# Kernel optimization log

Hardware: AMD Instinct MI355X
Metric: run time of the kernel (lower is better)

Reference implementation:

```python
import jax, jax.numpy as jnp
import numpy as np

CORE_DIM = 128
MEMORY_SLOTS = 64
B, S = 4, 4096


def setup_inputs() -> dict:
    key = jax.random.key(0)
    k1, k2, k3, k4, k5 = jax.random.split(key, 5)
    x = jax.random.normal(k1, (B, S, CORE_DIM), dtype=jnp.float32)
    memory_keys = jax.random.normal(k2, (MEMORY_SLOTS, CORE_DIM), dtype=jnp.float32)
    memory_ops = jax.random.normal(k3, (MEMORY_SLOTS, CORE_DIM, CORE_DIM), dtype=jnp.float32)
    # nn.Linear(core_dim, core_dim): weight [out, in], bias [out]
    bound = 1.0 / np.sqrt(CORE_DIM)
    Wq = jax.random.uniform(k4, (CORE_DIM, CORE_DIM), minval=-bound, maxval=bound, dtype=jnp.float32)
    bq = jax.random.uniform(k5, (CORE_DIM,), minval=-bound, maxval=bound, dtype=jnp.float32)
    return {"input_tensor": x, "memory_keys": memory_keys, "memory_ops": memory_ops, "Wq": Wq, "bq": bq}


def reference(input_tensor, memory_keys, memory_ops, Wq, bq):
    dim = input_tensor.shape[-1]
    # query projection: x @ Wq^T + bq
    queries = jnp.einsum('bsd,ed->bse', input_tensor, Wq) + bq
    # soft attention over memory slots
    attn_logits = jnp.einsum('bsd,md->bsm', queries, memory_keys)
    attn_weights = jax.nn.softmax(attn_logits / jnp.sqrt(jnp.float32(dim)), axis=-1)
    # fused: (sum_m attn[bsm] * ops[m]) @ x[bs]  == sum_m attn[bsm] * (ops[m] @ x[bs])
    processed = jnp.einsum('bsm,mde,bse->bsd', attn_weights, memory_ops, input_tensor)
    return processed
```

## Files before the change

### kernel.cpp

```cpp
#include <hip/hip_runtime.h>

typedef __bf16 bf16x8 __attribute__((ext_vector_type(8)));
typedef float f32x4 __attribute__((ext_vector_type(4)));
typedef unsigned int uint4v __attribute__((ext_vector_type(4)));
typedef unsigned short ushort_t;
typedef unsigned int uint_t;

#define RS 0.08838834764831845f

__device__ __forceinline__ ushort_t f2bf(float f) {
    uint_t u = __float_as_uint(f);
    u += 0x7FFFu + ((u >> 16) & 1u);
    return (ushort_t)(u >> 16);
}
__device__ __forceinline__ uint_t pack2(float a, float b) {
    return (uint_t)f2bf(a) | ((uint_t)f2bf(b) << 16);
}
union U4B8 { uint4v u; bf16x8 b; };
__device__ __forceinline__ bf16x8 as_bf(uint4v u) { U4B8 x; x.u = u; return x.b; }

__device__ __forceinline__ int xfrag(int f, int lane) {
    return f * 1072 + ((lane >> 4) * 272) + ((lane & 15) * 16);
}

__device__ __forceinline__ void gload16(const void* g, void* l) {
    __builtin_amdgcn_global_load_lds(
        (const __attribute__((address_space(1))) void*)g,
        (__attribute__((address_space(3))) void*)l, 16, 0, 0);
}

__global__ __launch_bounds__(256) void prep_kernel(
    const float* __restrict__ ops, const float* __restrict__ keys,
    const float* __restrict__ Wq, const float* __restrict__ bq,
    uint4v* __restrict__ ops_sw, ushort_t* __restrict__ kp_sw,
    float* __restrict__ cb)
{
    const int tid = threadIdx.x;
    const int b = blockIdx.x;
    if (b >= 64) {
        int g = (b - 64) * 256 + tid;
        int L = g & 63, dt = (g >> 6) & 7, ks = (g >> 9) & 3, m = g >> 11;
        int d = dt * 16 + (L & 15);
        int e0 = ks * 32 + ((L >> 4) << 3);
        const float4* s = (const float4*)(ops + (((size_t)(m * 128 + d)) << 7) + e0);
        float4 v0 = s[0], v1 = s[1];
        uint4v o = { pack2(v0.x, v0.y), pack2(v0.z, v0.w),
                     pack2(v1.x, v1.y), pack2(v1.z, v1.w) };
        int h = m * 2048 + (dt >> 2) * 1024 + ks * 256 + (dt & 3) * 64 + L;
        ops_sw[h] = o;
    } else {
        __shared__ float red[256];
        const int m = b;
        const int d = tid & 127, eh = tid >> 7;
        const float* kr = keys + m * 128 + eh * 64;
        const float* wc = Wq + (size_t)(eh * 64) * 128 + d;
        float acc = 0.f;
        #pragma unroll 8
        for (int e = 0; e < 64; ++e)
            acc = fmaf(kr[e], wc[(size_t)e * 128], acc);
        red[tid] = acc;
        __syncthreads();
        if (tid < 128) {
            float v = red[tid] + red[tid + 128];
            int ki = d >> 5, qq = (d >> 3) & 3, j = d & 7;
            kp_sw[((((ki * 4 + (m >> 4)) * 64) + (qq * 16 + (m & 15))) << 3) | j] = f2bf(v);
        } else if (tid >= 192) {
            int lane = tid - 192;
            float p = keys[m * 128 + lane] * bq[lane]
                    + keys[m * 128 + 64 + lane] * bq[64 + lane];
            #pragma unroll
            for (int off = 1; off < 64; off <<= 1) p += __shfl_xor(p, off);
            if (lane == 0) cb[m] = p;
        }
    }
}

__global__ __launch_bounds__(512, 2) void main_kernel(
    const float* __restrict__ x, const float* __restrict__ cb,
    const ushort_t* __restrict__ kp_sw, const uint4v* __restrict__ ops_sw,
    float* __restrict__ out)
{
    __shared__ __align__(16) unsigned char xs[34304];
    __shared__ float attn_f[64 * 132];
    __shared__ __align__(16) uint4v bb[2][2048];

    const int tid = threadIdx.x;
    const int lane = tid & 63;
    const int w = tid >> 6;
    const int q = lane >> 4;
    const int l15 = lane & 15;
    const int tb = blockIdx.x >> 1;
    const int dh = blockIdx.x & 1;
    const int t0 = tb * 128;
    const int dtp = w & 3;
    const int tg = w >> 2;

    {
        const float4* x4 = (const float4*)(x + (size_t)t0 * 128);
        #pragma unroll
        for (int it = 0; it < 4; ++it) {
            int i = it * 512 + tid;
            int t = i >> 4, kc = i & 15;
            float4 a = x4[t * 32 + kc * 2];
            float4 b2 = x4[t * 32 + kc * 2 + 1];
            uint4v o = { pack2(a.x, a.y), pack2(a.z, a.w),
                         pack2(b2.x, b2.y), pack2(b2.z, b2.w) };
            *(uint4v*)(xs + ((t >> 4) * 4 + (kc >> 2)) * 1072
                          + (kc & 3) * 272 + (t & 15) * 16) = o;
        }
    }
    __syncthreads();

    {
        f32x4 L0 = {0,0,0,0}, L1 = {0,0,0,0}, L2 = {0,0,0,0}, L3 = {0,0,0,0};
        const uint4v* kpf = (const uint4v*)kp_sw;
        #pragma unroll
        for (int ki = 0; ki < 4; ++ki) {
            bf16x8 a = *(const bf16x8*)(xs + xfrag(w * 4 + ki, lane));
            L0 = __builtin_amdgcn_mfma_f32_16x16x32_bf16(a, as_bf(kpf[(ki*4+0)*64 + lane]), L0, 0,0,0);
            L1 = __builtin_amdgcn_mfma_f32_16x16x32_bf16(a, as_bf(kpf[(ki*4+1)*64 + lane]), L1, 0,0,0);
            L2 = __builtin_amdgcn_mfma_f32_16x16x32_bf16(a, as_bf(kpf[(ki*4+2)*64 + lane]), L2, 0,0,0);
            L3 = __builtin_amdgcn_mfma_f32_16x16x32_bf16(a, as_bf(kpf[(ki*4+3)*64 + lane]), L3, 0,0,0);
        }
        float c0 = cb[l15], c1 = cb[16 + l15], c2 = cb[32 + l15], c3 = cb[48 + l15];
        #pragma unroll
        for (int r = 0; r < 4; ++r) {
            float v0 = (L0[r] + c0) * RS;
            float v1 = (L1[r] + c1) * RS;
            float v2 = (L2[r] + c2) * RS;
            float v3 = (L3[r] + c3) * RS;
            float mx = fmaxf(fmaxf(v0, v1), fmaxf(v2, v3));
            #pragma unroll
            for (int off = 1; off < 16; off <<= 1) mx = fmaxf(mx, __shfl_xor(mx, off));
            float e0 = __expf(v0 - mx), e1 = __expf(v1 - mx),
                  e2 = __expf(v2 - mx), e3 = __expf(v3 - mx);
            float sm = e0 + e1 + e2 + e3;
            #pragma unroll
            for (int off = 1; off < 16; off <<= 1) sm += __shfl_xor(sm, off);
            float inv = 1.0f / sm;
            int t = w * 16 + q * 4 + r;
            attn_f[(     l15) * 132 + t] = e0 * inv;
            attn_f[(16 + l15) * 132 + t] = e1 * inv;
            attn_f[(32 + l15) * 132 + t] = e2 * inv;
            attn_f[(48 + l15) * 132 + t] = e3 * inv;
        }
    }

    bf16x8 A[4][4];
    #pragma unroll
    for (int tf = 0; tf < 4; ++tf)
        #pragma unroll
        for (int ki = 0; ki < 4; ++ki)
            A[tf][ki] = *(const bf16x8*)(xs + xfrag(tg * 16 + tf * 4 + ki, lane));

    const int sb = w * 64 + lane;
    auto stage = [&](int pair, int buf) {
        #pragma unroll
        for (int j = 0; j < 4; ++j) {
            int slot = pair * 2 + (j >> 1);
            const uint4v* g = ops_sw + ((size_t)(slot * 2 + dh) << 10)
                            + (j & 1) * 512 + sb;
            gload16((const void*)g, (void*)&bb[buf][j * 512 + (w << 6)]);
        }
    };

    stage(0, 0);
    __syncthreads();

    f32x4 C[4] = {};
    #pragma unroll 2
    for (int p = 0; p < 32; ++p) {
        if (p < 31) stage(p + 1, (p + 1) & 1);
        const uint4v* bbuf = &bb[p & 1][0];
        #pragma unroll
        for (int sl = 0; sl < 2; ++sl) {
            const int m = p * 2 + sl;
            f32x4 S[4] = {};
            #pragma unroll
            for (int ki = 0; ki < 4; ++ki) {
                bf16x8 bfrag = as_bf(bbuf[sl * 1024 + ki * 256 + dtp * 64 + lane]);
                #pragma unroll
                for (int tf = 0; tf < 4; ++tf)
                    S[tf] = __builtin_amdgcn_mfma_f32_16x16x32_bf16(A[tf][ki], bfrag, S[tf], 0,0,0);
            }
            #pragma unroll
            for (int tf = 0; tf < 4; ++tf) {
                f32x4 af = *(const f32x4*)&attn_f[m * 132 + tg * 64 + tf * 16 + q * 4];
                #pragma unroll
                for (int r = 0; r < 4; ++r)
                    C[tf][r] = fmaf(af[r], S[tf][r], C[tf][r]);
            }
        }
        __syncthreads();
    }

    float* op = out + (size_t)t0 * 128 + dh * 64 + dtp * 16 + l15;
    #pragma unroll
    for (int tf = 0; tf < 4; ++tf)
        #pragma unroll
        for (int r = 0; r < 4; ++r)
            op[(size_t)(tg * 64 + tf * 16 + q * 4 + r) * 128] = C[tf][r];
}

extern "C" void kernel_launch(void* const* d_in, const int* in_sizes, int n_in,
                              void* d_out, int out_size, void* d_ws, size_t ws_size,
                              hipStream_t stream)
{
    const float* x    = (const float*)d_in[0];
    const float* keys = (const float*)d_in[1];
    const float* ops  = (const float*)d_in[2];
    const float* Wq   = (const float*)d_in[3];
    const float* bq   = (const float*)d_in[4];
    float* out = (float*)d_out;

    char* ws = (char*)d_ws;
    uint4v*   ops_sw = (uint4v*)ws;
    ushort_t* kp_sw  = (ushort_t*)(ws + 2097152);
    float*    cb     = (float*)(ws + 2097152 + 16384);

    prep_kernel<<<576, 256, 0, stream>>>(ops, keys, Wq, bq, ops_sw, kp_sw, cb);
    main_kernel<<<256, 512, 0, stream>>>(x, cb, kp_sw, ops_sw, out);
}
```

Measured before the change: 115.7 us.

## Triple-buffer ops staging with vmcnt waits and one barrier per pair

Puts all LDS into one buffer and reuses the x-staging region, once the A fragments are in registers, to hold three rotating ops buffers instead of two. Each iteration issues the next pair's loads, waits with s_waitcnt vmcnt(4) so only the older loads must finish, then takes one barrier. This removes the trailing __syncthreads and lets loads overlap compute. MFMA sections also raise wave priority with s_setprio. LDS use grows to about 129 KB, so the launch bound of 2 blocks per CU probably cannot be met and occupancy may drop.

Result: faster. 104.7 us (-9.5%).

```diff
diff --git a/kernel.cpp b/kernel.cpp
--- a/kernel.cpp
+++ b/kernel.cpp
@@ -80,9 +80,10 @@
     const ushort_t* __restrict__ kp_sw, const uint4v* __restrict__ ops_sw,
     float* __restrict__ out)
 {
-    __shared__ __align__(16) unsigned char xs[34304];
-    __shared__ float attn_f[64 * 132];
-    __shared__ __align__(16) uint4v bb[2][2048];
+    __shared__ __align__(16) unsigned char lds[132096];
+    float* attn_f = (float*)lds;
+    unsigned char* xs = lds + 33792;
+    uint4v* bb = (uint4v*)(lds + 33792);
 
     const int tid = threadIdx.x;
     const int lane = tid & 63;
@@ -153,36 +154,35 @@
         for (int ki = 0; ki < 4; ++ki)
             A[tf][ki] = *(const bf16x8*)(xs + xfrag(tg * 16 + tf * 4 + ki, lane));
 
-    const int sb = w * 64 + lane;
-    auto stage = [&](int pair, int buf) {
+    __syncthreads();
+
+    auto stage = [&](int pair, int b) {
+        uint4v* dst = bb + b * 2048 + w * 64;
+        const uint4v* src = ops_sw + (size_t)pair * 4096 + dh * 1024 + w * 64 + lane;
         #pragma unroll
         for (int j = 0; j < 4; ++j) {
-            int slot = pair * 2 + (j >> 1);
-            const uint4v* g = ops_sw + ((size_t)(slot * 2 + dh) << 10)
-                            + (j & 1) * 512 + sb;
-            gload16((const void*)g, (void*)&bb[buf][j * 512 + (w << 6)]);
+            const uint4v* g = src + (j >> 1) * 2048 + (j & 1) * 512;
+            gload16((const void*)g, (void*)(dst + j * 512));
         }
     };
 
-    stage(0, 0);
-    __syncthreads();
-
     f32x4 C[4] = {};
-    #pragma unroll 2
-    for (int p = 0; p < 32; ++p) {
-        if (p < 31) stage(p + 1, (p + 1) & 1);
-        const uint4v* bbuf = &bb[p & 1][0];
+
+    auto computePair = [&](int p) {
+        const uint4v* bbuf = bb + (p % 3) * 2048 + dtp * 64 + lane;
         #pragma unroll
         for (int sl = 0; sl < 2; ++sl) {
             const int m = p * 2 + sl;
             f32x4 S[4] = {};
+            __builtin_amdgcn_s_setprio(1);
             #pragma unroll
             for (int ki = 0; ki < 4; ++ki) {
-                bf16x8 bfrag = as_bf(bbuf[sl * 1024 + ki * 256 + dtp * 64 + lane]);
+                bf16x8 bfrag = as_bf(bbuf[sl * 1024 + ki * 256]);
                 #pragma unroll
                 for (int tf = 0; tf < 4; ++tf)
                     S[tf] = __builtin_amdgcn_mfma_f32_16x16x32_bf16(A[tf][ki], bfrag, S[tf], 0,0,0);
             }
+            __builtin_amdgcn_s_setprio(0);
             #pragma unroll
             for (int tf = 0; tf < 4; ++tf) {
                 f32x4 af = *(const f32x4*)&attn_f[m * 132 + tg * 64 + tf * 16 + q * 4];
@@ -191,8 +191,18 @@
                     C[tf][r] = fmaf(af[r], S[tf][r], C[tf][r]);
             }
         }
-        __syncthreads();
-    }
+    };
+
+    stage(0, 0);
+    for (int p = 0; p < 31; ++p) {
+        stage(p + 1, (p + 1) % 3);
+        asm volatile("s_waitcnt vmcnt(4)" ::: "memory");
+        __builtin_amdgcn_s_barrier();
+        computePair(p);
+    }
+    asm volatile("s_waitcnt vmcnt(0)" ::: "memory");
+    __builtin_amdgcn_s_barrier();
+    computePair(31);
 
     float* op = out + (size_t)t0 * 128 + dh * 64 + dtp * 16 + l15;
     #pragma unroll
```
